# Optimization experiments

Measured on AMD Instinct MI355X. Metric: run time of the kernel, lower is better.

Reference implementation:

```python
import jax, jax.numpy as jnp
import numpy as np

B, VOCAB, F = 4096, 50000, 64


def setup_inputs() -> dict:
    key = jax.random.key(0)
    k1, k2 = jax.random.split(key, 2)
    # binary multi-hot input (row > 0 mask semantics of the original)
    x = jax.random.randint(k1, (B, VOCAB), 0, 2, dtype=jnp.int32)
    # truncated-normal-ish init for the factor embedding table
    V = (jax.random.normal(k2, (VOCAB, F), dtype=jnp.float32) * 0.05)
    # linear (first-order) bias table is zero-initialized in the original
    bias = jnp.zeros((VOCAB, 1), dtype=jnp.float32)
    g_bias = jnp.zeros((), dtype=jnp.float32)
    return {"x": x, "V": V, "bias": bias, "g_bias": g_bias}


def reference(x, V, bias, g_bias):
    # x: [B, VOCAB] binary multi-hot; V: [VOCAB, F]; bias: [VOCAB, 1]; g_bias: scalar
    xf = x.astype(V.dtype)
    # FM sum-square identity: for selected rows S = {i : x_i > 0},
    # 0.5 * (sum_{i,j in S} <v_i, v_j> - sum_{i in S} ||v_i||^2)
    #   = 0.5 * (||sum_i v_i||^2 - sum_i ||v_i||^2)
    xv = xf @ V                                   # [B, F] = sum of selected rows
    sum_sq = jnp.sum(xv * xv, axis=-1)            # [B]
    sq_sum = xf @ jnp.sum(V * V, axis=-1)         # [B]
    second_order = 0.5 * (sum_sq - sq_sum)        # [B]
    linear = g_bias + xf @ bias                   # [B, 1]
    return linear + second_order[:, None]         # [B, 1]
```

## Files before the change

### kernel.cpp

```cpp
#include <hip/hip_runtime.h>

#define VOCAB 50000
#define BROWS 4096
#define F 64
#define NCOLS 80
#define NT 5
#define SPLITS 16
#define KT_PER_SPLIT 98
#define KT_TOTAL (SPLITS * KT_PER_SPLIT)
#define KPAD (KT_TOTAL * 32)

#define AS1 __attribute__((address_space(1)))
#define AS3 __attribute__((address_space(3)))

typedef __attribute__((ext_vector_type(4))) float f32x4;
typedef __attribute__((ext_vector_type(8))) short s16x8;

__device__ __forceinline__ unsigned short f2bf(float f) {
    unsigned u = __builtin_bit_cast(unsigned, f);
    unsigned r = (u + 0x7FFFu + ((u >> 16) & 1u)) >> 16;
    return (unsigned short)r;
}
__device__ __forceinline__ float bf2f(unsigned short b) {
    unsigned u = ((unsigned)b) << 16;
    return __builtin_bit_cast(float, u);
}

__global__ void fm_prep_w(const float* __restrict__ V, const float* __restrict__ bias,
                          float* __restrict__ w) {
    int k = blockIdx.x * blockDim.x + threadIdx.x;
    if (k >= KPAD) return;
    float val = 0.f;
    if (k < VOCAB) {
        const float4* row = reinterpret_cast<const float4*>(V + (size_t)k * F);
        float ss = 0.f;
#pragma unroll
        for (int j = 0; j < F / 4; ++j) {
            float4 v = row[j];
            ss += v.x * v.x + v.y * v.y + v.z * v.z + v.w * v.w;
        }
        val = bias[k] - 0.5f * ss;
    }
    w[k] = val;
}

__global__ void fm_prep_bfrag(const float* __restrict__ V, const float* __restrict__ w,
                              uint4* __restrict__ bfrag) {
    int t = blockIdx.x * blockDim.x + threadIdx.x;
    if (t >= KT_TOTAL * NT * 64) return;
    int lane = t & 63;
    int tile = t >> 6;
    int nt = tile % NT;
    int kt = tile / NT;
    int n = nt * 16 + (lane & 15);
    int kbase = kt * 32 + (lane >> 4) * 8;
    unsigned short o[8];
#pragma unroll
    for (int j = 0; j < 8; ++j) {
        int k = kbase + j;
        float v = 0.f;
        if (k < VOCAB) {
            if (n < F) {
                v = V[(size_t)k * F + n];
            } else if (n == F) {
                v = w[k];
            } else if (n == F + 1) {
                float wv = w[k];
                v = wv - bf2f(f2bf(wv));
            }
        }
        o[j] = f2bf(v);
    }
    uint4 pk;
    pk.x = (unsigned)o[0] | ((unsigned)o[1] << 16);
    pk.y = (unsigned)o[2] | ((unsigned)o[3] << 16);
    pk.z = (unsigned)o[4] | ((unsigned)o[5] << 16);
    pk.w = (unsigned)o[6] | ((unsigned)o[7] << 16);
    bfrag[t] = pk;
}

__global__ __launch_bounds__(256, 4) void fm_main(const int* __restrict__ x,
                                                  const uint4* __restrict__ bfrag,
                                                  float* __restrict__ part) {
    __shared__ uint4 bbuf[2][NT * 64];
    const int bx = blockIdx.x;
    const int split = bx & (SPLITS - 1);
    const int mblock = bx >> 4;
    const int tid = threadIdx.x;
    const int wave = tid >> 6;
    const int lane = tid & 63;
    const int kb = lane >> 4;
    const int rowA = mblock * 64 + wave * 16 + (lane & 15);
    const int* __restrict__ xrow = x + (size_t)rowA * VOCAB;
    const int kt0 = split * KT_PER_SPLIT;

    auto stage = [&](int buf, int kt) {
        const uint4* src = bfrag + (size_t)kt * (NT * 64);
        __builtin_amdgcn_global_load_lds(
            (const AS1 void*)(src + (wave << 6) + lane),
            (AS3 void*)(&bbuf[buf][wave << 6]), 16, 0, 0);
        if (wave == 0)
            __builtin_amdgcn_global_load_lds(
                (const AS1 void*)(src + 256 + lane),
                (AS3 void*)(&bbuf[buf][256]), 16, 0, 0);
    };

    f32x4 acc[NT];
#pragma unroll
    for (int nt = 0; nt < NT; ++nt) acc[nt] = (f32x4){0.f, 0.f, 0.f, 0.f};

    stage(0, kt0);
    __syncthreads();
    int cur = 0;

    const int nfull = (split == SPLITS - 1) ? (((VOCAB - 32) >> 5) + 1 - kt0) : KT_PER_SPLIT;

    int it = 0;
    for (; it < nfull; ++it) {
        if (it + 1 < KT_PER_SPLIT) stage(cur ^ 1, kt0 + it + 1);
        const int k = (kt0 + it) * 32 + kb * 8;
        int4 a0 = *reinterpret_cast<const int4*>(xrow + k);
        int4 a1 = *reinterpret_cast<const int4*>(xrow + k + 4);
        uint4 apk;
        apk.x = ((unsigned)a0.x + ((unsigned)a0.y << 16)) * 16256u;
        apk.y = ((unsigned)a0.z + ((unsigned)a0.w << 16)) * 16256u;
        apk.z = ((unsigned)a1.x + ((unsigned)a1.y << 16)) * 16256u;
        apk.w = ((unsigned)a1.z + ((unsigned)a1.w << 16)) * 16256u;
        s16x8 afrag = __builtin_bit_cast(s16x8, apk);
#pragma unroll
        for (int nt = 0; nt < NT; ++nt) {
            s16x8 bf = __builtin_bit_cast(s16x8, bbuf[cur][nt * 64 + lane]);
            acc[nt] = __builtin_amdgcn_mfma_f32_16x16x32_bf16(afrag, bf, acc[nt], 0, 0, 0);
        }
        __syncthreads();
        cur ^= 1;
    }
    for (; it < KT_PER_SPLIT; ++it) {
        if (it + 1 < KT_PER_SPLIT) stage(cur ^ 1, kt0 + it + 1);
        const int k = (kt0 + it) * 32 + kb * 8;
        unsigned xv[8];
#pragma unroll
        for (int j = 0; j < 8; ++j) xv[j] = (k + j < VOCAB) ? (unsigned)xrow[k + j] : 0u;
        uint4 apk;
        apk.x = (xv[0] + (xv[1] << 16)) * 16256u;
        apk.y = (xv[2] + (xv[3] << 16)) * 16256u;
        apk.z = (xv[4] + (xv[5] << 16)) * 16256u;
        apk.w = (xv[6] + (xv[7] << 16)) * 16256u;
        s16x8 afrag = __builtin_bit_cast(s16x8, apk);
#pragma unroll
        for (int nt = 0; nt < NT; ++nt) {
            s16x8 bf = __builtin_bit_cast(s16x8, bbuf[cur][nt * 64 + lane]);
            acc[nt] = __builtin_amdgcn_mfma_f32_16x16x32_bf16(afrag, bf, acc[nt], 0, 0, 0);
        }
        __syncthreads();
        cur ^= 1;
    }

    float* __restrict__ p = part + (size_t)split * BROWS * NCOLS;
    int m0 = mblock * 64 + wave * 16 + kb * 4;
    int c0 = lane & 15;
#pragma unroll
    for (int nt = 0; nt < NT; ++nt)
#pragma unroll
        for (int r = 0; r < 4; ++r)
            p[(size_t)(m0 + r) * NCOLS + nt * 16 + c0] = acc[nt][r];
}

__global__ void fm_reduce(const float* __restrict__ part, const float* __restrict__ gbias,
                          float* __restrict__ out) {
    int b = blockIdx.x * 4 + (threadIdx.x >> 6);
    int lane = threadIdx.x & 63;
    float acc = 0.f;
#pragma unroll
    for (int s = 0; s < SPLITS; ++s)
        acc += part[((size_t)s * BROWS + b) * NCOLS + lane];
    float sq = acc * acc;
    float ex = 0.f;
    if (lane < 16)       ex = part[((size_t)lane * BROWS + b) * NCOLS + F];
    else if (lane < 32)  ex = part[((size_t)(lane - 16) * BROWS + b) * NCOLS + F + 1];
#pragma unroll
    for (int off = 32; off; off >>= 1) {
        sq += __shfl_xor(sq, off, 64);
        ex += __shfl_xor(ex, off, 64);
    }
    if (lane == 0) out[b] = gbias[0] + ex + 0.5f * sq;
}

extern "C" void kernel_launch(void* const* d_in, const int* in_sizes, int n_in,
                              void* d_out, int out_size, void* d_ws, size_t ws_size,
                              hipStream_t stream) {
    const int*   x     = (const int*)d_in[0];
    const float* V     = (const float*)d_in[1];
    const float* bias  = (const float*)d_in[2];
    const float* gbias = (const float*)d_in[3];
    float* out = (float*)d_out;

    char* ws = (char*)d_ws;
    uint4* bfrag = (uint4*)ws;
    float* w     = (float*)(ws + (size_t)KT_TOTAL * NT * 64 * 16);
    float* part  = (float*)(ws + (size_t)KT_TOTAL * NT * 64 * 16 + (size_t)KPAD * 4);

    fm_prep_w<<<(KPAD + 255) / 256, 256, 0, stream>>>(V, bias, w);
    fm_prep_bfrag<<<(KT_TOTAL * NT * 64 + 255) / 256, 256, 0, stream>>>(V, w, bfrag);
    fm_main<<<(BROWS / 64) * SPLITS, 256, 0, stream>>>(x, bfrag, part);
    fm_reduce<<<BROWS / 4, 256, 0, stream>>>(part, gbias, out);
}
```

Measured before the change: 201.6 us.

## Process two k-tiles per round and software-prefetch x into registers

The main loop now stages two 32-wide k-tiles of B fragments per LDS buffer and runs 10 MFMAs per barrier, which halves the number of __syncthreads. The x loads for the next round are issued into registers before the current round's MFMAs, so global latency on the dominant x stream overlaps with compute. The cost is higher register pressure from the extra prefetched int4 values and double the LDS per block, which may reduce occupancy under launch_bounds(256,4). The tail split switches to guarded loads from round 46.

Result: slower. 232.8 us (+15.5%).

```diff
diff --git a/kernel.cpp b/kernel.cpp
--- a/kernel.cpp
+++ b/kernel.cpp
@@ -7,6 +7,7 @@
 #define NT 5
 #define SPLITS 16
 #define KT_PER_SPLIT 98
+#define NR 49
 #define KT_TOTAL (SPLITS * KT_PER_SPLIT)
 #define KPAD (KT_TOTAL * 32)
 
@@ -82,7 +83,7 @@
 __global__ __launch_bounds__(256, 4) void fm_main(const int* __restrict__ x,
                                                   const uint4* __restrict__ bfrag,
                                                   float* __restrict__ part) {
-    __shared__ uint4 bbuf[2][NT * 64];
+    __shared__ uint4 bbuf[2][2 * NT * 64];
     const int bx = blockIdx.x;
     const int split = bx & (SPLITS - 1);
     const int mblock = bx >> 4;
@@ -93,67 +94,78 @@
     const int rowA = mblock * 64 + wave * 16 + (lane & 15);
     const int* __restrict__ xrow = x + (size_t)rowA * VOCAB;
     const int kt0 = split * KT_PER_SPLIT;
-
-    auto stage = [&](int buf, int kt) {
-        const uint4* src = bfrag + (size_t)kt * (NT * 64);
-        __builtin_amdgcn_global_load_lds(
-            (const AS1 void*)(src + (wave << 6) + lane),
-            (AS3 void*)(&bbuf[buf][wave << 6]), 16, 0, 0);
-        if (wave == 0)
-            __builtin_amdgcn_global_load_lds(
-                (const AS1 void*)(src + 256 + lane),
-                (AS3 void*)(&bbuf[buf][256]), 16, 0, 0);
-    };
-
-    f32x4 acc[NT];
-#pragma unroll
-    for (int nt = 0; nt < NT; ++nt) acc[nt] = (f32x4){0.f, 0.f, 0.f, 0.f};
-
-    stage(0, kt0);
-    __syncthreads();
-    int cur = 0;
-
-    const int nfull = (split == SPLITS - 1) ? (((VOCAB - 32) >> 5) + 1 - kt0) : KT_PER_SPLIT;
-
-    int it = 0;
-    for (; it < nfull; ++it) {
-        if (it + 1 < KT_PER_SPLIT) stage(cur ^ 1, kt0 + it + 1);
-        const int k = (kt0 + it) * 32 + kb * 8;
-        int4 a0 = *reinterpret_cast<const int4*>(xrow + k);
-        int4 a1 = *reinterpret_cast<const int4*>(xrow + k + 4);
+    const int e0 = (wave << 6) + lane;
+
+    auto stage = [&](int buf, int rnd) {
+        const uint4* src = bfrag + (size_t)(kt0 + 2 * rnd) * (NT * 64);
+        __builtin_amdgcn_global_load_lds((const AS1 void*)(src + e0),
+                                         (AS3 void*)(&bbuf[buf][wave << 6]), 16, 0, 0);
+        __builtin_amdgcn_global_load_lds((const AS1 void*)(src + 256 + e0),
+                                         (AS3 void*)(&bbuf[buf][256 + (wave << 6)]), 16, 0, 0);
+        if (wave < 2)
+            __builtin_amdgcn_global_load_lds((const AS1 void*)(src + 512 + e0),
+                                             (AS3 void*)(&bbuf[buf][512 + (wave << 6)]), 16, 0, 0);
+    };
+    auto loadx = [&](int rnd, int4* dst) {
+        const int k = (kt0 + 2 * rnd) * 32 + kb * 8;
+        dst[0] = *reinterpret_cast<const int4*>(xrow + k);
+        dst[1] = *reinterpret_cast<const int4*>(xrow + k + 4);
+        dst[2] = *reinterpret_cast<const int4*>(xrow + k + 32);
+        dst[3] = *reinterpret_cast<const int4*>(xrow + k + 36);
+    };
+    auto loadx_g = [&](int rnd, int4* dst) {
+        const int k = (kt0 + 2 * rnd) * 32 + kb * 8;
+        int v[16];
+#pragma unroll
+        for (int j = 0; j < 8; ++j) v[j] = (k + j < VOCAB) ? xrow[k + j] : 0;
+#pragma unroll
+        for (int j = 0; j < 8; ++j) v[8 + j] = (k + 32 + j < VOCAB) ? xrow[k + 32 + j] : 0;
+        dst[0] = make_int4(v[0], v[1], v[2], v[3]);
+        dst[1] = make_int4(v[4], v[5], v[6], v[7]);
+        dst[2] = make_int4(v[8], v[9], v[10], v[11]);
+        dst[3] = make_int4(v[12], v[13], v[14], v[15]);
+    };
+    auto mk = [&](int4 a0, int4 a1) -> s16x8 {
         uint4 apk;
         apk.x = ((unsigned)a0.x + ((unsigned)a0.y << 16)) * 16256u;
         apk.y = ((unsigned)a0.z + ((unsigned)a0.w << 16)) * 16256u;
         apk.z = ((unsigned)a1.x + ((unsigned)a1.y << 16)) * 16256u;
         apk.w = ((unsigned)a1.z + ((unsigned)a1.w << 16)) * 16256u;
-        s16x8 afrag = __builtin_bit_cast(s16x8, apk);
+        return __builtin_bit_cast(s16x8, apk);
+    };
+
+    f32x4 acc[NT];
+#pragma unroll
+    for (int nt = 0; nt < NT; ++nt) acc[nt] = (f32x4){0.f, 0.f, 0.f, 0.f};
+
+    int4 xr[4], nx[4];
+    stage(0, 0);
+    loadx(0, xr);
+    __syncthreads();
+
+    const int nfast = (split == SPLITS - 1) ? 46 : NR;
+    int buf = 0;
+    for (int r = 0; r < NR; ++r) {
+        if (r + 1 < NR) {
+            stage(buf ^ 1, r + 1);
+            if (r + 1 < nfast) loadx(r + 1, nx);
+            else               loadx_g(r + 1, nx);
+        }
+        s16x8 af0 = mk(xr[0], xr[1]);
+        s16x8 af1 = mk(xr[2], xr[3]);
 #pragma unroll
         for (int nt = 0; nt < NT; ++nt) {
-            s16x8 bf = __builtin_bit_cast(s16x8, bbuf[cur][nt * 64 + lane]);
-            acc[nt] = __builtin_amdgcn_mfma_f32_16x16x32_bf16(afrag, bf, acc[nt], 0, 0, 0);
+            s16x8 b0 = __builtin_bit_cast(s16x8, bbuf[buf][nt * 64 + lane]);
+            acc[nt] = __builtin_amdgcn_mfma_f32_16x16x32_bf16(af0, b0, acc[nt], 0, 0, 0);
+        }
+#pragma unroll
+        for (int nt = 0; nt < NT; ++nt) {
+            s16x8 b1 = __builtin_bit_cast(s16x8, bbuf[buf][320 + nt * 64 + lane]);
+            acc[nt] = __builtin_amdgcn_mfma_f32_16x16x32_bf16(af1, b1, acc[nt], 0, 0, 0);
         }
         __syncthreads();
-        cur ^= 1;
-    }
-    for (; it < KT_PER_SPLIT; ++it) {
-        if (it + 1 < KT_PER_SPLIT) stage(cur ^ 1, kt0 + it + 1);
-        const int k = (kt0 + it) * 32 + kb * 8;
-        unsigned xv[8];
-#pragma unroll
-        for (int j = 0; j < 8; ++j) xv[j] = (k + j < VOCAB) ? (unsigned)xrow[k + j] : 0u;
-        uint4 apk;
-        apk.x = (xv[0] + (xv[1] << 16)) * 16256u;
-        apk.y = (xv[2] + (xv[3] << 16)) * 16256u;
-        apk.z = (xv[4] + (xv[5] << 16)) * 16256u;
-        apk.w = (xv[6] + (xv[7] << 16)) * 16256u;
-        s16x8 afrag = __builtin_bit_cast(s16x8, apk);
-#pragma unroll
-        for (int nt = 0; nt < NT; ++nt) {
-            s16x8 bf = __builtin_bit_cast(s16x8, bbuf[cur][nt * 64 + lane]);
-            acc[nt] = __builtin_amdgcn_mfma_f32_16x16x32_bf16(afrag, bf, acc[nt], 0, 0, 0);
-        }
-        __syncthreads();
-        cur ^= 1;
+        xr[0] = nx[0]; xr[1] = nx[1]; xr[2] = nx[2]; xr[3] = nx[3];
+        buf ^= 1;
     }
 
     float* __restrict__ p = part + (size_t)split * BROWS * NCOLS;
```

## Prefetch x tiles one iteration ahead with a single barrier per step

Applied to the files above, without the earlier changes.

Restructures the main MFMA loop so the next K-tile of the multi-hot input x is loaded into registers one iteration ahead, overlapping it with the current MFMAs. The end-of-iteration __syncthreads is replaced by one s_barrier at the top of each step, after an explicit vmcnt wait for the LDS staging. The block-to-split mapping is also permuted to change how splits are spread across the GPU. The bounds-checked tail for the last split is handled separately. This raises register pressure and depends on hand-written wait counts being correct.

New measurement: 209.1 us. +3.7%, slower.

```diff
diff --git a/kernel.cpp b/kernel.cpp
--- a/kernel.cpp
+++ b/kernel.cpp
@@ -6,8 +6,8 @@
 #define NCOLS 80
 #define NT 5
 #define SPLITS 16
-#define KT_PER_SPLIT 98
-#define KT_TOTAL (SPLITS * KT_PER_SPLIT)
+#define NR 98
+#define KT_TOTAL (SPLITS * NR)
 #define KPAD (KT_TOTAL * 32)
 
 #define AS1 __attribute__((address_space(1)))
@@ -83,77 +83,93 @@
                                                   const uint4* __restrict__ bfrag,
                                                   float* __restrict__ part) {
     __shared__ uint4 bbuf[2][NT * 64];
-    const int bx = blockIdx.x;
-    const int split = bx & (SPLITS - 1);
-    const int mblock = bx >> 4;
+    const int bid = blockIdx.x;
+    const int split = (bid & 7) * 2 + ((bid >> 3) & 1);
+    const int mblock = bid >> 4;
     const int tid = threadIdx.x;
     const int wave = tid >> 6;
     const int lane = tid & 63;
     const int kb = lane >> 4;
     const int rowA = mblock * 64 + wave * 16 + (lane & 15);
     const int* __restrict__ xrow = x + (size_t)rowA * VOCAB;
-    const int kt0 = split * KT_PER_SPLIT;
-
-    auto stage = [&](int buf, int kt) {
-        const uint4* src = bfrag + (size_t)kt * (NT * 64);
-        __builtin_amdgcn_global_load_lds(
-            (const AS1 void*)(src + (wave << 6) + lane),
-            (AS3 void*)(&bbuf[buf][wave << 6]), 16, 0, 0);
+    const int kt0 = split * NR;
+    const int e0 = (wave << 6) + lane;
+
+    auto stage = [&](int rnd) {
+        const uint4* src = bfrag + (size_t)(kt0 + rnd) * (NT * 64);
+        uint4* dst = bbuf[rnd & 1];
+        __builtin_amdgcn_global_load_lds((const AS1 void*)(src + e0),
+                                         (AS3 void*)(dst + (wave << 6)), 16, 0, 0);
         if (wave == 0)
-            __builtin_amdgcn_global_load_lds(
-                (const AS1 void*)(src + 256 + lane),
-                (AS3 void*)(&bbuf[buf][256]), 16, 0, 0);
+            __builtin_amdgcn_global_load_lds((const AS1 void*)(src + 256 + lane),
+                                             (AS3 void*)(dst + 256), 16, 0, 0);
     };
-
-    f32x4 acc[NT];
-#pragma unroll
-    for (int nt = 0; nt < NT; ++nt) acc[nt] = (f32x4){0.f, 0.f, 0.f, 0.f};
-
-    stage(0, kt0);
-    __syncthreads();
-    int cur = 0;
-
-    const int nfull = (split == SPLITS - 1) ? (((VOCAB - 32) >> 5) + 1 - kt0) : KT_PER_SPLIT;
-
-    int it = 0;
-    for (; it < nfull; ++it) {
-        if (it + 1 < KT_PER_SPLIT) stage(cur ^ 1, kt0 + it + 1);
-        const int k = (kt0 + it) * 32 + kb * 8;
-        int4 a0 = *reinterpret_cast<const int4*>(xrow + k);
-        int4 a1 = *reinterpret_cast<const int4*>(xrow + k + 4);
+    auto mk = [&](int4 a0, int4 a1) -> s16x8 {
         uint4 apk;
         apk.x = ((unsigned)a0.x + ((unsigned)a0.y << 16)) * 16256u;
         apk.y = ((unsigned)a0.z + ((unsigned)a0.w << 16)) * 16256u;
         apk.z = ((unsigned)a1.x + ((unsigned)a1.y << 16)) * 16256u;
         apk.w = ((unsigned)a1.z + ((unsigned)a1.w << 16)) * 16256u;
-        s16x8 afrag = __builtin_bit_cast(s16x8, apk);
+        return __builtin_bit_cast(s16x8, apk);
+    };
+
+    f32x4 acc[NT];
+#pragma unroll
+    for (int nt = 0; nt < NT; ++nt) acc[nt] = (f32x4){0.f, 0.f, 0.f, 0.f};
+
+    int4 xa, xb, na, nb;
+    stage(0);
+    {
+        const int k = kt0 * 32 + kb * 8;
+        xa = *reinterpret_cast<const int4*>(xrow + k);
+        xb = *reinterpret_cast<const int4*>(xrow + k + 4);
+    }
+
+    const int nfast = (split == SPLITS - 1) ? 91 : NR;
+
+    for (int r = 0; r < nfast; ++r) {
+        asm volatile("s_waitcnt vmcnt(2)");
+        __builtin_amdgcn_sched_barrier(0);
+        __builtin_amdgcn_s_barrier();
+        __builtin_amdgcn_sched_barrier(0);
+        if (r + 1 < nfast) {
+            stage(r + 1);
+            const int k = (kt0 + r + 1) * 32 + kb * 8;
+            na = *reinterpret_cast<const int4*>(xrow + k);
+            nb = *reinterpret_cast<const int4*>(xrow + k + 4);
+        }
+        s16x8 af = mk(xa, xb);
+        const uint4* bb = bbuf[r & 1];
 #pragma unroll
         for (int nt = 0; nt < NT; ++nt) {
-            s16x8 bf = __builtin_bit_cast(s16x8, bbuf[cur][nt * 64 + lane]);
-            acc[nt] = __builtin_amdgcn_mfma_f32_16x16x32_bf16(afrag, bf, acc[nt], 0, 0, 0);
-        }
-        __syncthreads();
-        cur ^= 1;
-    }
-    for (; it < KT_PER_SPLIT; ++it) {
-        if (it + 1 < KT_PER_SPLIT) stage(cur ^ 1, kt0 + it + 1);
-        const int k = (kt0 + it) * 32 + kb * 8;
-        unsigned xv[8];
-#pragma unroll
-        for (int j = 0; j < 8; ++j) xv[j] = (k + j < VOCAB) ? (unsigned)xrow[k + j] : 0u;
-        uint4 apk;
-        apk.x = (xv[0] + (xv[1] << 16)) * 16256u;
-        apk.y = (xv[2] + (xv[3] << 16)) * 16256u;
-        apk.z = (xv[4] + (xv[5] << 16)) * 16256u;
-        apk.w = (xv[6] + (xv[7] << 16)) * 16256u;
-        s16x8 afrag = __builtin_bit_cast(s16x8, apk);
-#pragma unroll
-        for (int nt = 0; nt < NT; ++nt) {
-            s16x8 bf = __builtin_bit_cast(s16x8, bbuf[cur][nt * 64 + lane]);
-            acc[nt] = __builtin_amdgcn_mfma_f32_16x16x32_bf16(afrag, bf, acc[nt], 0, 0, 0);
-        }
-        __syncthreads();
-        cur ^= 1;
+            s16x8 bf = __builtin_bit_cast(s16x8, bb[nt * 64 + lane]);
+            acc[nt] = __builtin_amdgcn_mfma_f32_16x16x32_bf16(af, bf, acc[nt], 0, 0, 0);
+        }
+        xa = na; xb = nb;
+    }
+
+    if (split == SPLITS - 1) {
+        for (int t = nfast; t < NR; ++t) {
+            if (t == nfast) stage(t);
+            const int k = (kt0 + t) * 32 + kb * 8;
+            unsigned xv[8];
+#pragma unroll
+            for (int j = 0; j < 8; ++j) xv[j] = (k + j < VOCAB) ? (unsigned)xrow[k + j] : 0u;
+            __syncthreads();
+            uint4 apk;
+            apk.x = (xv[0] + (xv[1] << 16)) * 16256u;
+            apk.y = (xv[2] + (xv[3] << 16)) * 16256u;
+            apk.z = (xv[4] + (xv[5] << 16)) * 16256u;
+            apk.w = (xv[6] + (xv[7] << 16)) * 16256u;
+            s16x8 af = __builtin_bit_cast(s16x8, apk);
+            const uint4* bb = bbuf[t & 1];
+#pragma unroll
+            for (int nt = 0; nt < NT; ++nt) {
+                s16x8 bf = __builtin_bit_cast(s16x8, bb[nt * 64 + lane]);
+                acc[nt] = __builtin_amdgcn_mfma_f32_16x16x32_bf16(af, bf, acc[nt], 0, 0, 0);
+            }
+            if (t + 1 < NR) stage(t + 1);
+        }
     }
 
     float* __restrict__ p = part + (size_t)split * BROWS * NCOLS;
```
